# Kernel optimization log

Measured on AMD Instinct MI355X. Metric: run time of the kernel, lower is better.

Reference implementation:

```python
import jax, jax.numpy as jnp
import numpy as np

SCALE = 64.0
MARGIN = 0.35
LAMBDA = 0.4
GAMMA = 2
EPS = 1e-12


def _l2_normalize(v, axis=-1):
    n = jnp.sqrt(jnp.sum(v * v, axis=axis, keepdims=True))
    return v / jnp.maximum(n, EPS)


def setup_inputs() -> dict:
    key = jax.random.key(0)
    k1, k2, k3, k4 = jax.random.split(key, 4)
    B, D, C = 1024, 512, 100000
    stdv = 1.0 / np.sqrt(D)
    x = jax.random.normal(k1, (B, D), dtype=jnp.float32)
    target = jax.random.randint(k2, (B,), 0, C, dtype=jnp.int64)
    id_agent = jax.random.uniform(k3, (C, D), dtype=jnp.float32, minval=-stdv, maxval=stdv)
    b = jax.random.uniform(k4, (C, D), dtype=jnp.float32, minval=-stdv, maxval=stdv)
    return {"x": x, "target": target, "id_agent": id_agent, "b": b}


def reference(x, target, id_agent, b):
    B = x.shape[0]
    x_n = _l2_normalize(x, axis=1)              # [B, D]
    w = _l2_normalize(id_agent, axis=1)         # [C, D] (in-place normalize in torch)

    # discriminative loss
    w_batch = w[target]                          # [B, D] gather
    d = x_n - w_batch                            # displacement vectors
    bt = b[target]                               # [B, D]
    bt_norm = jnp.sqrt(jnp.sum(bt * bt, axis=1, keepdims=True))
    bt_norm_c = jnp.clip(bt_norm, 0.0, 0.05)
    bt_unit = bt / jnp.maximum(bt_norm, EPS)
    resid = d - bt_unit * bt_norm_c
    loss_disc = jnp.mean(jnp.sqrt(jnp.sum(resid * resid, axis=1)))

    # AM-softmax logits with margin on target class (training mode)
    score = x_n @ w.T                            # [B, C] large GEMM
    rows = jnp.arange(B)
    score = score.at[rows, target].add(-MARGIN)
    score = score * SCALE

    # focal cross-entropy: CE mean first, then focal modulation (as in source)
    logsm = jax.nn.log_softmax(score, axis=1)
    nll = -logsm[rows, target]
    logp = jnp.mean(nll)
    p = jnp.exp(-logp)
    loss_score = (1.0 - p) ** GAMMA * logp

    return (LAMBDA * loss_disc + loss_score)[None]  # shape [1]
```

## Files before the change

kernel.cpp:

```cpp
#include <hip/hip_runtime.h>
#include <hip/hip_bf16.h>

typedef __attribute__((ext_vector_type(4))) int i32x4;

#define B_N 1024
#define D_K 512
#define C_N 100000
#define SCALE_F 64.0f
#define MARGIN_F 0.35f
#define BM 128
#define BN 128
#define BKB 128
#define NT_ 782
#define MT_ 8
#define MAXL 64.0f
#define KQ (SCALE_F / (127.0f * 127.0f))

__device__ __forceinline__ float dot4(float4 a, float4 b) {
    return a.x * b.x + a.y * b.y + a.z * b.z + a.w * b.w;
}
__device__ __forceinline__ float amax4(float4 a) {
    return fmaxf(fmaxf(fabsf(a.x), fabsf(a.y)), fmaxf(fabsf(a.z), fabsf(a.w)));
}
__device__ __forceinline__ int packq(float v0, float v1, float v2, float v3, float qs) {
    int q0 = __float2int_rn(v0 * qs), q1 = __float2int_rn(v1 * qs);
    int q2 = __float2int_rn(v2 * qs), q3 = __float2int_rn(v3 * qs);
    return (q0 & 0xFF) | ((q1 & 0xFF) << 8) | ((q2 & 0xFF) << 16) | ((q3 & 0xFF) << 24);
}

__global__ void normx_disc_kernel(const float* __restrict__ x,
                                  const int* __restrict__ target,
                                  const float* __restrict__ ida,
                                  const float* __restrict__ bmat,
                                  char* __restrict__ xq,
                                  float* __restrict__ sx,
                                  float* __restrict__ sums,
                                  float* __restrict__ tlogit) {
    int row = blockIdx.x * 4 + (threadIdx.x >> 6);
    int l = threadIdx.x & 63;
    long t = (long)target[row];
    const float4* xp = (const float4*)(x + (size_t)row * D_K);
    const float4* wp = (const float4*)(ida + (size_t)t * D_K);
    const float4* bp = (const float4*)(bmat + (size_t)t * D_K);
    float4 x0 = xp[l], x1 = xp[64 + l];
    float4 w0 = wp[l], w1 = wp[64 + l];
    float4 b0 = bp[l], b1 = bp[64 + l];
    float xssq = dot4(x0, x0) + dot4(x1, x1);
    float wssq = dot4(w0, w0) + dot4(w1, w1);
    float bssq = dot4(b0, b0) + dot4(b1, b1);
    float xmx = fmaxf(amax4(x0), amax4(x1));
#pragma unroll
    for (int m = 1; m < 64; m <<= 1) {
        xssq += __shfl_xor(xssq, m);
        wssq += __shfl_xor(wssq, m);
        bssq += __shfl_xor(bssq, m);
        xmx = fmaxf(xmx, __shfl_xor(xmx, m));
    }
    float xinv = 1.0f / fmaxf(sqrtf(xssq), 1e-12f);
    float winv = 1.0f / fmaxf(sqrtf(wssq), 1e-12f);
    float btn = sqrtf(bssq);
    float cs = fminf(btn, 0.05f) / fmaxf(btn, 1e-12f);

    float sxm = fmaxf(xmx * xinv, 1e-12f);
    float qs = 127.0f / sxm * xinv;
    int* oq = (int*)(xq + (size_t)row * D_K);
    oq[l] = packq(x0.x, x0.y, x0.z, x0.w, qs);
    oq[64 + l] = packq(x1.x, x1.y, x1.z, x1.w, qs);
    if (l == 0) sx[row] = sxm;

    float xs[8] = {x0.x, x0.y, x0.z, x0.w, x1.x, x1.y, x1.z, x1.w};
    float wv[8] = {w0.x, w0.y, w0.z, w0.w, w1.x, w1.y, w1.z, w1.w};
    float bv[8] = {b0.x, b0.y, b0.z, b0.w, b1.x, b1.y, b1.z, b1.w};
    float rss = 0.0f, dt = 0.0f;
#pragma unroll
    for (int i = 0; i < 8; ++i) {
        float xn = xs[i] * xinv;
        float wn = wv[i] * winv;
        float d = xn - wn;
        float r = d - bv[i] * cs;
        rss += r * r;
        dt += xn * wn;
    }
#pragma unroll
    for (int m = 1; m < 64; m <<= 1) {
        rss += __shfl_xor(rss, m);
        dt += __shfl_xor(dt, m);
    }
    if (l == 0) {
        atomicAdd(&sums[0], sqrtf(rss));
        tlogit[row] = SCALE_F * dt;
    }
}

__global__ void norm_w_kernel(const float* __restrict__ w,
                              char* __restrict__ wq,
                              float* __restrict__ sw) {
    int row = blockIdx.x * 4 + (threadIdx.x >> 6);
    int l = threadIdx.x & 63;
    const float4* rp = (const float4*)(w + (size_t)row * D_K);
    float4 a = rp[l], b = rp[64 + l];
    float ssq = dot4(a, a) + dot4(b, b);
    float mx = fmaxf(amax4(a), amax4(b));
#pragma unroll
    for (int m = 1; m < 64; m <<= 1) {
        ssq += __shfl_xor(ssq, m);
        mx = fmaxf(mx, __shfl_xor(mx, m));
    }
    float inv = 1.0f / fmaxf(sqrtf(ssq), 1e-12f);
    float swm = fmaxf(mx * inv, 1e-12f);
    float qs = 127.0f / swm * inv;
    int* oq = (int*)(wq + (size_t)row * D_K);
    oq[l] = packq(a.x, a.y, a.z, a.w, qs);
    oq[64 + l] = packq(b.x, b.y, b.z, b.w, qs);
    if (l == 0) sw[row] = swm;
}

__global__ __launch_bounds__(256, 4) void gemm_lse_kernel(const char* __restrict__ A,
                                                          const char* __restrict__ W,
                                                          const float* __restrict__ sx,
                                                          const float* __restrict__ sw,
                                                          float* __restrict__ rowsum) {
    __shared__ char As[BM * BKB];
    __shared__ char Bs[BN * BKB];
    __shared__ float sxl[BM];
    __shared__ float swl[BN];
    __shared__ float rs[2][BM];

    int tid = threadIdx.x;
    int wave = tid >> 6, l = tid & 63;
    int wm = wave >> 1, wn = wave & 1;

    int tile = (blockIdx.x & 7) * NT_ + (blockIdx.x >> 3);
    int nt = tile >> 3, mt = tile & 7;
    int m0 = mt * BM, n0 = nt * BN;

    int srow = l >> 3;
    int scolB = ((l & 7) ^ (l >> 3)) * 16;

    if (tid < BM) {
        sxl[tid] = sx[m0 + tid];
        int c = n0 + tid;
        swl[tid] = sw[c < C_N ? c : C_N - 1];
    }

    i32x4 acc[4][4];
#pragma unroll
    for (int i = 0; i < 4; ++i)
#pragma unroll
        for (int j = 0; j < 4; ++j) acc[i][j] = (i32x4){0, 0, 0, 0};

    int cl = l & 15, hi = l >> 4;

    for (int kt = 0; kt < 4; ++kt) {
#pragma unroll
        for (int i = 0; i < 4; ++i) {
            int rb = wave * 32 + i * 8;
            const char* ga = A + (size_t)(m0 + rb + srow) * D_K + kt * BKB + scolB;
            __builtin_amdgcn_global_load_lds(
                (const __attribute__((address_space(1))) void*)ga,
                (__attribute__((address_space(3))) void*)&As[rb * BKB], 16, 0, 0);
            int rn = n0 + rb + srow;
            rn = rn < C_N ? rn : C_N - 1;
            const char* gb = W + (size_t)rn * D_K + kt * BKB + scolB;
            __builtin_amdgcn_global_load_lds(
                (const __attribute__((address_space(1))) void*)gb,
                (__attribute__((address_space(3))) void*)&Bs[rb * BKB], 16, 0, 0);
        }
        __syncthreads();

#pragma unroll
        for (int kk = 0; kk < 2; ++kk) {
            int px = (((kk << 2) | hi) ^ (cl & 7)) * 16;
            i32x4 af[4], bfr[4];
#pragma unroll
            for (int mi = 0; mi < 4; ++mi)
                af[mi] = *(const i32x4*)&As[(wm * 64 + mi * 16 + cl) * BKB + px];
#pragma unroll
            for (int ni = 0; ni < 4; ++ni)
                bfr[ni] = *(const i32x4*)&Bs[(wn * 64 + ni * 16 + cl) * BKB + px];
#pragma unroll
            for (int mi = 0; mi < 4; ++mi)
#pragma unroll
                for (int ni = 0; ni < 4; ++ni)
                    acc[mi][ni] = __builtin_amdgcn_mfma_i32_16x16x64_i8(af[mi], bfr[ni], acc[mi][ni], 0, 0, 0);
        }
        __syncthreads();
    }

    float frv[4][4], fcv[4];
#pragma unroll
    for (int mi = 0; mi < 4; ++mi)
#pragma unroll
        for (int j = 0; j < 4; ++j)
            frv[mi][j] = sxl[wm * 64 + mi * 16 + hi * 4 + j] * KQ;
#pragma unroll
    for (int ni = 0; ni < 4; ++ni)
        fcv[ni] = swl[wn * 64 + ni * 16 + cl];

#pragma unroll
    for (int mi = 0; mi < 4; ++mi) {
#pragma unroll
        for (int j = 0; j < 4; ++j) {
            float se = 0.0f;
#pragma unroll
            for (int ni = 0; ni < 4; ++ni) {
                int cg = n0 + wn * 64 + ni * 16 + cl;
                if (cg < C_N)
                    se += __expf((float)acc[mi][ni][j] * frv[mi][j] * fcv[ni] - MAXL);
            }
#pragma unroll
            for (int xm = 1; xm < 16; xm <<= 1) se += __shfl_xor(se, xm);
            if (cl == 0) rs[wn][wm * 64 + mi * 16 + hi * 4 + j] = se;
        }
    }
    __syncthreads();
    if (tid < BM) {
        float s = rs[0][tid] + rs[1][tid];
        atomicAdd(&rowsum[m0 + tid], s);
    }
}

__global__ void rowfin_final_kernel(const float* __restrict__ rowsum,
                                    const float* __restrict__ tlogit,
                                    const float* __restrict__ sums,
                                    float* __restrict__ out) {
    __shared__ float red[16];
    int tid = threadIdx.x;
    float lse = MAXL + logf(rowsum[tid]);
    float st = tlogit[tid];
    float corr = __expf(st - lse) * (__expf(-SCALE_F * MARGIN_F) - 1.0f);
    float lse2 = lse + log1pf(corr);
    float nll = lse2 - (st - SCALE_F * MARGIN_F);
#pragma unroll
    for (int xm = 1; xm < 64; xm <<= 1) nll += __shfl_xor(nll, xm);
    if ((tid & 63) == 0) red[tid >> 6] = nll;
    __syncthreads();
    if (tid == 0) {
        float s = 0.0f;
#pragma unroll
        for (int i = 0; i < 16; ++i) s += red[i];
        float logp = s * (1.0f / B_N);
        float disc = sums[0] * (1.0f / B_N);
        float p = __expf(-logp);
        float om = 1.0f - p;
        out[0] = 0.4f * disc + om * om * logp;
    }
}

extern "C" void kernel_launch(void* const* d_in, const int* in_sizes, int n_in,
                              void* d_out, int out_size, void* d_ws, size_t ws_size,
                              hipStream_t stream) {
    const float* x = (const float*)d_in[0];
    const int* target = (const int*)d_in[1];
    const float* ida = (const float*)d_in[2];
    const float* bmat = (const float*)d_in[3];
    float* out = (float*)d_out;

    char* ws = (char*)d_ws;
    size_t off = 0;
    float* rowsum = (float*)(ws + off);  off += (size_t)B_N * 4;
    float* sums = (float*)(ws + off);    off += 256;
    char* xq = (char*)(ws + off);        off += (size_t)B_N * D_K;
    char* wq = (char*)(ws + off);        off += (size_t)C_N * D_K;
    float* sx = (float*)(ws + off);      off += (size_t)B_N * 4;
    float* sw = (float*)(ws + off);      off += (size_t)C_N * 4;
    float* tlogit = (float*)(ws + off);  off += (size_t)B_N * 4;

    hipMemsetAsync(rowsum, 0, (size_t)B_N * 4 + 256, stream);

    normx_disc_kernel<<<B_N / 4, 256, 0, stream>>>(x, target, ida, bmat, xq, sx, sums, tlogit);
    norm_w_kernel<<<C_N / 4, 256, 0, stream>>>(ida, wq, sw);
    gemm_lse_kernel<<<MT_ * NT_, 256, 0, stream>>>(xq, wq, sx, sw, rowsum);
    rowfin_final_kernel<<<1, 1024, 0, stream>>>(rowsum, tlogit, sums, out);
}
```

Measured before the change: 149.4 us.

## Switch int8 GEMM to 32x32x32 MFMA tiles and drop memset launch

The GEMM inner loop moves from 16x16x64 int8 MFMA on a 4x4 fragment grid to 32x32x32 int8 MFMA on a 2x2 grid. The aim is fewer LDS fragment loads per MFMA and fewer epilogue shuffle reductions. The hipMemsetAsync and the atomic disc-loss accumulation are removed: rowsum is now zeroed in the first kernel, and per-row disc values are reduced in the final kernel. The epilogue reduction now spans 32 lanes, and the accumulator register layout changes, so the row mapping has to be correct.

```diff
diff --git a/kernel.cpp b/kernel.cpp
--- a/kernel.cpp
+++ b/kernel.cpp
@@ -2,6 +2,7 @@
 #include <hip/hip_bf16.h>
 
 typedef __attribute__((ext_vector_type(4))) int i32x4;
+typedef __attribute__((ext_vector_type(16))) int i32x16;
 
 #define B_N 1024
 #define D_K 512
@@ -34,8 +35,9 @@
                                   const float* __restrict__ bmat,
                                   char* __restrict__ xq,
                                   float* __restrict__ sx,
-                                  float* __restrict__ sums,
-                                  float* __restrict__ tlogit) {
+                                  float* __restrict__ dpart,
+                                  float* __restrict__ tlogit,
+                                  float* __restrict__ rowsum) {
     int row = blockIdx.x * 4 + (threadIdx.x >> 6);
     int l = threadIdx.x & 63;
     long t = (long)target[row];
@@ -66,7 +68,6 @@
     int* oq = (int*)(xq + (size_t)row * D_K);
     oq[l] = packq(x0.x, x0.y, x0.z, x0.w, qs);
     oq[64 + l] = packq(x1.x, x1.y, x1.z, x1.w, qs);
-    if (l == 0) sx[row] = sxm;
 
     float xs[8] = {x0.x, x0.y, x0.z, x0.w, x1.x, x1.y, x1.z, x1.w};
     float wv[8] = {w0.x, w0.y, w0.z, w0.w, w1.x, w1.y, w1.z, w1.w};
@@ -87,8 +88,10 @@
         dt += __shfl_xor(dt, m);
     }
     if (l == 0) {
-        atomicAdd(&sums[0], sqrtf(rss));
+        sx[row] = sxm;
+        dpart[row] = sqrtf(rss);
         tlogit[row] = SCALE_F * dt;
+        rowsum[row] = 0.0f;
     }
 }
 
@@ -143,13 +146,15 @@
         swl[tid] = sw[c < C_N ? c : C_N - 1];
     }
 
-    i32x4 acc[4][4];
-#pragma unroll
-    for (int i = 0; i < 4; ++i)
-#pragma unroll
-        for (int j = 0; j < 4; ++j) acc[i][j] = (i32x4){0, 0, 0, 0};
-
-    int cl = l & 15, hi = l >> 4;
+    i32x16 acc[2][2];
+#pragma unroll
+    for (int i = 0; i < 2; ++i)
+#pragma unroll
+        for (int j = 0; j < 2; ++j)
+#pragma unroll
+            for (int e = 0; e < 16; ++e) acc[i][j][e] = 0;
+
+    int l31 = l & 31, hi5 = l >> 5;
 
     for (int kt = 0; kt < 4; ++kt) {
 #pragma unroll
@@ -169,48 +174,46 @@
         __syncthreads();
 
 #pragma unroll
-        for (int kk = 0; kk < 2; ++kk) {
-            int px = (((kk << 2) | hi) ^ (cl & 7)) * 16;
-            i32x4 af[4], bfr[4];
-#pragma unroll
-            for (int mi = 0; mi < 4; ++mi)
-                af[mi] = *(const i32x4*)&As[(wm * 64 + mi * 16 + cl) * BKB + px];
-#pragma unroll
-            for (int ni = 0; ni < 4; ++ni)
-                bfr[ni] = *(const i32x4*)&Bs[(wn * 64 + ni * 16 + cl) * BKB + px];
-#pragma unroll
-            for (int mi = 0; mi < 4; ++mi)
-#pragma unroll
-                for (int ni = 0; ni < 4; ++ni)
-                    acc[mi][ni] = __builtin_amdgcn_mfma_i32_16x16x64_i8(af[mi], bfr[ni], acc[mi][ni], 0, 0, 0);
+        for (int ks = 0; ks < 4; ++ks) {
+            int px = (((ks << 1) | hi5) ^ (l & 7)) * 16;
+            i32x4 af[2], bfr[2];
+#pragma unroll
+            for (int mi = 0; mi < 2; ++mi)
+                af[mi] = *(const i32x4*)&As[(wm * 64 + mi * 32 + l31) * BKB + px];
+#pragma unroll
+            for (int ni = 0; ni < 2; ++ni)
+                bfr[ni] = *(const i32x4*)&Bs[(wn * 64 + ni * 32 + l31) * BKB + px];
+#pragma unroll
+            for (int mi = 0; mi < 2; ++mi)
+#pragma unroll
+                for (int ni = 0; ni < 2; ++ni)
+                    acc[mi][ni] = __builtin_amdgcn_mfma_i32_32x32x32_i8(af[mi], bfr[ni], acc[mi][ni], 0, 0, 0);
         }
         __syncthreads();
     }
 
-    float frv[4][4], fcv[4];
-#pragma unroll
-    for (int mi = 0; mi < 4; ++mi)
-#pragma unroll
-        for (int j = 0; j < 4; ++j)
-            frv[mi][j] = sxl[wm * 64 + mi * 16 + hi * 4 + j] * KQ;
-#pragma unroll
-    for (int ni = 0; ni < 4; ++ni)
-        fcv[ni] = swl[wn * 64 + ni * 16 + cl];
-
-#pragma unroll
-    for (int mi = 0; mi < 4; ++mi) {
-#pragma unroll
-        for (int j = 0; j < 4; ++j) {
+    float fcv[2];
+#pragma unroll
+    for (int ni = 0; ni < 2; ++ni)
+        fcv[ni] = swl[wn * 64 + ni * 32 + l31];
+    bool cok[2];
+#pragma unroll
+    for (int ni = 0; ni < 2; ++ni)
+        cok[ni] = (n0 + wn * 64 + ni * 32 + l31) < C_N;
+
+#pragma unroll
+    for (int mi = 0; mi < 2; ++mi) {
+#pragma unroll
+        for (int reg = 0; reg < 16; ++reg) {
+            int rloc = mi * 32 + (reg & 3) + 8 * (reg >> 2) + 4 * hi5;
+            float fr = sxl[wm * 64 + rloc] * KQ;
             float se = 0.0f;
 #pragma unroll
-            for (int ni = 0; ni < 4; ++ni) {
-                int cg = n0 + wn * 64 + ni * 16 + cl;
-                if (cg < C_N)
-                    se += __expf((float)acc[mi][ni][j] * frv[mi][j] * fcv[ni] - MAXL);
-            }
-#pragma unroll
-            for (int xm = 1; xm < 16; xm <<= 1) se += __shfl_xor(se, xm);
-            if (cl == 0) rs[wn][wm * 64 + mi * 16 + hi * 4 + j] = se;
+            for (int ni = 0; ni < 2; ++ni)
+                if (cok[ni]) se += __expf((float)acc[mi][ni][reg] * fr * fcv[ni] - MAXL);
+#pragma unroll
+            for (int xm = 1; xm < 32; xm <<= 1) se += __shfl_xor(se, xm);
+            if (l31 == 0) rs[wn][wm * 64 + rloc] = se;
         }
     }
     __syncthreads();
@@ -222,25 +225,33 @@
 
 __global__ void rowfin_final_kernel(const float* __restrict__ rowsum,
                                     const float* __restrict__ tlogit,
-                                    const float* __restrict__ sums,
+                                    const float* __restrict__ dpart,
                                     float* __restrict__ out) {
-    __shared__ float red[16];
+    __shared__ float redn[16];
+    __shared__ float redd[16];
     int tid = threadIdx.x;
     float lse = MAXL + logf(rowsum[tid]);
     float st = tlogit[tid];
     float corr = __expf(st - lse) * (__expf(-SCALE_F * MARGIN_F) - 1.0f);
     float lse2 = lse + log1pf(corr);
     float nll = lse2 - (st - SCALE_F * MARGIN_F);
-#pragma unroll
-    for (int xm = 1; xm < 64; xm <<= 1) nll += __shfl_xor(nll, xm);
-    if ((tid & 63) == 0) red[tid >> 6] = nll;
+    float dv = dpart[tid];
+#pragma unroll
+    for (int xm = 1; xm < 64; xm <<= 1) {
+        nll += __shfl_xor(nll, xm);
+        dv += __shfl_xor(dv, xm);
+    }
+    if ((tid & 63) == 0) {
+        redn[tid >> 6] = nll;
+        redd[tid >> 6] = dv;
+    }
     __syncthreads();
     if (tid == 0) {
-        float s = 0.0f;
-#pragma unroll
-        for (int i = 0; i < 16; ++i) s += red[i];
-        float logp = s * (1.0f / B_N);
-        float disc = sums[0] * (1.0f / B_N);
+        float sn = 0.0f, sd = 0.0f;
+#pragma unroll
+        for (int i = 0; i < 16; ++i) { sn += redn[i]; sd += redd[i]; }
+        float logp = sn * (1.0f / B_N);
+        float disc = sd * (1.0f / B_N);
         float p = __expf(-logp);
         float om = 1.0f - p;
         out[0] = 0.4f * disc + om * om * logp;
@@ -259,17 +270,15 @@
     char* ws = (char*)d_ws;
     size_t off = 0;
     float* rowsum = (float*)(ws + off);  off += (size_t)B_N * 4;
-    float* sums = (float*)(ws + off);    off += 256;
     char* xq = (char*)(ws + off);        off += (size_t)B_N * D_K;
     char* wq = (char*)(ws + off);        off += (size_t)C_N * D_K;
     float* sx = (float*)(ws + off);      off += (size_t)B_N * 4;
     float* sw = (float*)(ws + off);      off += (size_t)C_N * 4;
     float* tlogit = (float*)(ws + off);  off += (size_t)B_N * 4;
-
-    hipMemsetAsync(rowsum, 0, (size_t)B_N * 4 + 256, stream);
-
-    normx_disc_kernel<<<B_N / 4, 256, 0, stream>>>(x, target, ida, bmat, xq, sx, sums, tlogit);
+    float* dpart = (float*)(ws + off);   off += (size_t)B_N * 4;
+
+    normx_disc_kernel<<<B_N / 4, 256, 0, stream>>>(x, target, ida, bmat, xq, sx, dpart, tlogit, rowsum);
     norm_w_kernel<<<C_N / 4, 256, 0, stream>>>(ida, wq, sw);
     gemm_lse_kernel<<<MT_ * NT_, 256, 0, stream>>>(xq, wq, sx, sw, rowsum);
-    rowfin_final_kernel<<<1, 1024, 0, stream>>>(rowsum, tlogit, sums, out);
-}
+    rowfin_final_kernel<<<1, 1024, 0, stream>>>(rowsum, tlogit, dpart, out);
+}
```

After: 163.3 us. 9.3% more time.
